# Kernel tuning notes

Hardware: AMD Instinct MI355X
Metric: run time of the kernel (lower is better)

Reference implementation:

```python
import jax, jax.numpy as jnp
import numpy as np

D = 768
N_GROUPS = 4
KEYS_PER_Q = 4 * 196  # 784


def setup_inputs() -> dict:
    key = jax.random.key(0)
    ks = jax.random.split(key, 6)
    scale = 0.02
    return {
        "LR_image": jax.random.normal(ks[0], (N_GROUPS, 32, D), jnp.float32),
        "HR_image": jax.random.normal(ks[1], (N_GROUPS, 32 * KEYS_PER_Q, D), jnp.float32),
        "Wq": jax.random.normal(ks[2], (D, D), jnp.float32) * scale,
        "bq": jnp.zeros((D,), jnp.float32),
        "Wk": jax.random.normal(ks[3], (D, D), jnp.float32) * scale,
        "bk": jnp.zeros((D,), jnp.float32),
        "Wv": jax.random.normal(ks[4], (D, D), jnp.float32) * scale,
        "bv": jnp.zeros((D,), jnp.float32),
        "Wo": jax.random.normal(ks[5], (D, D), jnp.float32) * scale,
        "bo": jnp.zeros((D,), jnp.float32),
        "gamma": jnp.ones((D,), jnp.float32),
        "beta": jnp.zeros((D,), jnp.float32),
    }


def reference(LR_image, HR_image, Wq, bq, Wk, bk, Wv, bv, Wo, bo, gamma, beta):
    d = LR_image.shape[-1]
    # version == 2 reshapes from the original forward
    lr = LR_image.reshape(1, -1, 32, 1, d)            # [1, N, 32, 1, D]
    hr = HR_image.reshape(1, -1, 32, KEYS_PER_Q, d)   # [1, N, 32, 784, D]
    q = lr @ Wq.T + bq                                # [1, N, 32, 1, D]
    k = hr @ Wk.T + bk                                # [1, N, 32, 784, D]
    v = hr @ Wv.T + bv
    # single-head attention; query_len == 1, key_len == 784
    scores = jnp.einsum('bnsqd,bnskd->bnsqk', q, k) / jnp.sqrt(jnp.float32(d))
    p = jax.nn.softmax(scores, axis=-1)               # dropout = identity (eval)
    x = jnp.einsum('bnsqk,bnskd->bnsqd', p, v)        # [1, N, 32, 1, D]
    x = x.reshape(1, -1, d)                           # [1, N*32, D]
    q = q.reshape(1, -1, d)
    x = x @ Wo.T + bo
    y = q + x                                         # residual (dropout_2 = identity)
    mu = jnp.mean(y, axis=-1, keepdims=True)
    var = jnp.mean((y - mu) ** 2, axis=-1, keepdims=True)
    return (y - mu) * jax.lax.rsqrt(var + 1e-5) * gamma + beta
```

## Files before the change

kernel.cpp:

```cpp
#include <hip/hip_runtime.h>
#include <math.h>

#define D 768
#define DF2 384
#define DF4 192
#define NQ 128
#define KPQ 784
#define NCHUNK 16
#define KCHUNK 49

#define EXP2F(x) __builtin_amdgcn_exp2f(x)

__device__ __forceinline__ float dot4f(const float4 a, const float4 b) {
    return a.x * b.x + a.y * b.y + a.z * b.z + a.w * b.w;
}

__global__ __launch_bounds__(256) void k_tr(const float* __restrict__ Wq,
                                            const float* __restrict__ Wv,
                                            const float* __restrict__ Wo,
                                            float* __restrict__ WqT,
                                            float* __restrict__ WvT,
                                            float* __restrict__ WoT) {
    __shared__ float t[64][65];
    const float* src;
    float* dst;
    if (blockIdx.y == 0)      { src = Wq; dst = WqT; }
    else if (blockIdx.y == 1) { src = Wv; dst = WvT; }
    else                      { src = Wo; dst = WoT; }
    const int tr = blockIdx.x / 12, tc = blockIdx.x % 12;
    const int r0 = tr * 64, c0 = tc * 64;
    const int lr = threadIdx.x >> 6, lc = threadIdx.x & 63;
#pragma unroll
    for (int i = 0; i < 16; ++i)
        t[lr + i * 4][lc] = src[(size_t)(r0 + lr + i * 4) * D + c0 + lc];
    __syncthreads();
#pragma unroll
    for (int i = 0; i < 16; ++i)
        dst[(size_t)(c0 + lr + i * 4) * D + r0 + lc] = t[lc][lr + i * 4];
}

template <bool BIAS, bool RES, bool SCALE>
__global__ __launch_bounds__(512) void k_gemm2(const float* __restrict__ A,
                                               const float2* __restrict__ W2,
                                               const float2* __restrict__ bias2,
                                               const float2* __restrict__ res2,
                                               float2* __restrict__ Out2) {
    __shared__ float2 part[8][4][64];
    const int ct  = blockIdx.x % 6;
    const int q0  = (blockIdx.x / 6) * 4;
    const int tid = threadIdx.x;
    const int ds  = __builtin_amdgcn_readfirstlane(tid >> 6);
    const int c2  = tid & 63;
    const int e2  = ct * 64 + c2;
    const float* a0 = A + (size_t)q0 * D;
    const float* a1 = a0 + D;
    const float* a2 = a1 + D;
    const float* a3 = a2 + D;
    float2 acc0 = {0.f, 0.f}, acc1 = {0.f, 0.f}, acc2 = {0.f, 0.f}, acc3 = {0.f, 0.f};
    const int dbase = ds * 96;
#pragma unroll 8
    for (int i = 0; i < 96; ++i) {
        const int d = dbase + i;
        const float2 wv = W2[(size_t)d * DF2 + e2];
        const float x0 = a0[d], x1 = a1[d], x2 = a2[d], x3 = a3[d];
        acc0.x = fmaf(x0, wv.x, acc0.x); acc0.y = fmaf(x0, wv.y, acc0.y);
        acc1.x = fmaf(x1, wv.x, acc1.x); acc1.y = fmaf(x1, wv.y, acc1.y);
        acc2.x = fmaf(x2, wv.x, acc2.x); acc2.y = fmaf(x2, wv.y, acc2.y);
        acc3.x = fmaf(x3, wv.x, acc3.x); acc3.y = fmaf(x3, wv.y, acc3.y);
    }
    part[ds][0][c2] = acc0;
    part[ds][1][c2] = acc1;
    part[ds][2][c2] = acc2;
    part[ds][3][c2] = acc3;
    __syncthreads();
    if (tid < 256) {
        const int q = tid >> 6, c = tid & 63;
        float2 s = {0.f, 0.f};
#pragma unroll
        for (int p = 0; p < 8; ++p) {
            s.x += part[p][q][c].x;
            s.y += part[p][q][c].y;
        }
        if (BIAS) {
            const float2 b = bias2[ct * 64 + c];
            s.x += b.x; s.y += b.y;
        }
        if (RES) {
            const float2 r = res2[(size_t)(q0 + q) * DF2 + ct * 64 + c];
            s.x += r.x; s.y += r.y;
        }
        if (SCALE) {
            const float rsd2 = 0.036084391824351615f * 1.4426950408889634f;
            s.x *= rsd2; s.y *= rsd2;
        }
        Out2[(size_t)(q0 + q) * DF2 + ct * 64 + c] = s;
    }
}

__global__ __launch_bounds__(256) void k_flash(const float4* __restrict__ HR,
                                               const float4* __restrict__ qt,
                                               float4* __restrict__ Cpart,
                                               float* __restrict__ Lp) {
    const int b     = blockIdx.x;
    const int qi    = b >> 4;
    const int chunk = b & 15;
    const size_t rowbase = (size_t)qi * KPQ + (size_t)chunk * KCHUNK;
    const int tid  = threadIdx.x;
    const int w    = tid >> 6;
    const int lane = tid & 63;

    const float4 qa = qt[qi * DF4 + lane];
    const float4 qb = qt[qi * DF4 + lane + 64];
    const float4 qc = qt[qi * DF4 + lane + 128];

    float l = 0.f;
    float4 c0 = make_float4(0.f, 0.f, 0.f, 0.f);
    float4 c1 = make_float4(0.f, 0.f, 0.f, 0.f);
    float4 c2 = make_float4(0.f, 0.f, 0.f, 0.f);

    int j = w;
    while (j + 12 < KCHUNK) {
        const float4* rA = HR + (rowbase + (size_t)j) * DF4;
        const float4* rB = HR + (rowbase + (size_t)(j + 4)) * DF4;
        const float4* rF = HR + (rowbase + (size_t)(j + 8)) * DF4;
        const float4* rG = HR + (rowbase + (size_t)(j + 12)) * DF4;
        const float4 a0 = rA[lane], a1 = rA[lane + 64], a2 = rA[lane + 128];
        const float4 b0 = rB[lane], b1 = rB[lane + 64], b2 = rB[lane + 128];
        const float4 f0 = rF[lane], f1 = rF[lane + 64], f2 = rF[lane + 128];
        const float4 g0 = rG[lane], g1 = rG[lane + 64], g2 = rG[lane + 128];
        float p1 = dot4f(qa, a0) + dot4f(qb, a1) + dot4f(qc, a2);
        float p2 = dot4f(qa, b0) + dot4f(qb, b1) + dot4f(qc, b2);
        float p3 = dot4f(qa, f0) + dot4f(qb, f1) + dot4f(qc, f2);
        float p4 = dot4f(qa, g0) + dot4f(qb, g1) + dot4f(qc, g2);
#pragma unroll
        for (int off = 32; off; off >>= 1) {
            p1 += __shfl_xor(p1, off, 64);
            p2 += __shfl_xor(p2, off, 64);
            p3 += __shfl_xor(p3, off, 64);
            p4 += __shfl_xor(p4, off, 64);
        }
        const float e1 = EXP2F(p1);
        const float e2 = EXP2F(p2);
        const float e3 = EXP2F(p3);
        const float e4 = EXP2F(p4);
        l += (e1 + e2) + (e3 + e4);
        c0.x = fmaf(e1, a0.x, fmaf(e2, b0.x, fmaf(e3, f0.x, fmaf(e4, g0.x, c0.x))));
        c0.y = fmaf(e1, a0.y, fmaf(e2, b0.y, fmaf(e3, f0.y, fmaf(e4, g0.y, c0.y))));
        c0.z = fmaf(e1, a0.z, fmaf(e2, b0.z, fmaf(e3, f0.z, fmaf(e4, g0.z, c0.z))));
        c0.w = fmaf(e1, a0.w, fmaf(e2, b0.w, fmaf(e3, f0.w, fmaf(e4, g0.w, c0.w))));
        c1.x = fmaf(e1, a1.x, fmaf(e2, b1.x, fmaf(e3, f1.x, fmaf(e4, g1.x, c1.x))));
        c1.y = fmaf(e1, a1.y, fmaf(e2, b1.y, fmaf(e3, f1.y, fmaf(e4, g1.y, c1.y))));
        c1.z = fmaf(e1, a1.z, fmaf(e2, b1.z, fmaf(e3, f1.z, fmaf(e4, g1.z, c1.z))));
        c1.w = fmaf(e1, a1.w, fmaf(e2, b1.w, fmaf(e3, f1.w, fmaf(e4, g1.w, c1.w))));
        c2.x = fmaf(e1, a2.x, fmaf(e2, b2.x, fmaf(e3, f2.x, fmaf(e4, g2.x, c2.x))));
        c2.y = fmaf(e1, a2.y, fmaf(e2, b2.y, fmaf(e3, f2.y, fmaf(e4, g2.y, c2.y))));
        c2.z = fmaf(e1, a2.z, fmaf(e2, b2.z, fmaf(e3, f2.z, fmaf(e4, g2.z, c2.z))));
        c2.w = fmaf(e1, a2.w, fmaf(e2, b2.w, fmaf(e3, f2.w, fmaf(e4, g2.w, c2.w))));
        j += 16;
    }
    while (j < KCHUNK) {
        const float4* rA = HR + (rowbase + (size_t)j) * DF4;
        const float4 a0 = rA[lane], a1 = rA[lane + 64], a2 = rA[lane + 128];
        float p1 = dot4f(qa, a0) + dot4f(qb, a1) + dot4f(qc, a2);
#pragma unroll
        for (int off = 32; off; off >>= 1) p1 += __shfl_xor(p1, off, 64);
        const float e1 = EXP2F(p1);
        l += e1;
        c0.x = fmaf(e1, a0.x, c0.x); c0.y = fmaf(e1, a0.y, c0.y);
        c0.z = fmaf(e1, a0.z, c0.z); c0.w = fmaf(e1, a0.w, c0.w);
        c1.x = fmaf(e1, a1.x, c1.x); c1.y = fmaf(e1, a1.y, c1.y);
        c1.z = fmaf(e1, a1.z, c1.z); c1.w = fmaf(e1, a1.w, c1.w);
        c2.x = fmaf(e1, a2.x, c2.x); c2.y = fmaf(e1, a2.y, c2.y);
        c2.z = fmaf(e1, a2.z, c2.z); c2.w = fmaf(e1, a2.w, c2.w);
        j += 4;
    }

    __shared__ __align__(16) float4 c_lds[4][DF4];
    __shared__ float l_lds[4];
    c_lds[w][lane]       = c0;
    c_lds[w][lane + 64]  = c1;
    c_lds[w][lane + 128] = c2;
    if (lane == 0) l_lds[w] = l;
    __syncthreads();

    if (tid < DF4) {
        float4 cc = make_float4(0.f, 0.f, 0.f, 0.f);
#pragma unroll
        for (int p = 0; p < 4; ++p) {
            const float4 cv = c_lds[p][tid];
            cc.x += cv.x; cc.y += cv.y; cc.z += cv.z; cc.w += cv.w;
        }
        Cpart[(size_t)b * DF4 + tid] = cc;
        if (tid == 0) Lp[b] = l_lds[0] + l_lds[1] + l_lds[2] + l_lds[3];
    }
}

__global__ __launch_bounds__(192) void k_combine(const float4* __restrict__ Cpart,
                                                 const float* __restrict__ Lp,
                                                 float4* __restrict__ Cn) {
    const int qi = blockIdx.x;
    const int f  = threadIdx.x;
    float L = 0.f;
#pragma unroll
    for (int p = 0; p < NCHUNK; ++p) L += Lp[qi * NCHUNK + p];
    float4 c = make_float4(0.f, 0.f, 0.f, 0.f);
#pragma unroll
    for (int p = 0; p < NCHUNK; ++p) {
        const float4 v = Cpart[(size_t)(qi * NCHUNK + p) * DF4 + f];
        c.x += v.x; c.y += v.y; c.z += v.z; c.w += v.w;
    }
    const float inv = 1.f / L;
    c.x *= inv; c.y *= inv; c.z *= inv; c.w *= inv;
    Cn[(size_t)qi * DF4 + f] = c;
}

__global__ __launch_bounds__(256) void k_ln(const float* __restrict__ y,
                                            const float* __restrict__ gamma,
                                            const float* __restrict__ beta,
                                            float* __restrict__ out) {
    __shared__ float sp[4], ssp[4];
    const int qi = blockIdx.x;
    const int tid = threadIdx.x, w = tid >> 6, lane = tid & 63;
    const float* yr = y + (size_t)qi * D;
    const float v0 = yr[tid], v1 = yr[tid + 256], v2 = yr[tid + 512];
    float s  = v0 + v1 + v2;
    float ss = v0 * v0 + v1 * v1 + v2 * v2;
#pragma unroll
    for (int off = 32; off; off >>= 1) {
        s  += __shfl_xor(s, off, 64);
        ss += __shfl_xor(ss, off, 64);
    }
    if (lane == 0) { sp[w] = s; ssp[w] = ss; }
    __syncthreads();
    s  = sp[0] + sp[1] + sp[2] + sp[3];
    ss = ssp[0] + ssp[1] + ssp[2] + ssp[3];
    const float mu  = s * (1.f / 768.f);
    const float var = ss * (1.f / 768.f) - mu * mu;
    const float rs  = rsqrtf(var + 1e-5f);
    float* o = out + (size_t)qi * D;
    o[tid]       = (v0 - mu) * rs * gamma[tid]       + beta[tid];
    o[tid + 256] = (v1 - mu) * rs * gamma[tid + 256] + beta[tid + 256];
    o[tid + 512] = (v2 - mu) * rs * gamma[tid + 512] + beta[tid + 512];
}

extern "C" void kernel_launch(void* const* d_in, const int* in_sizes, int n_in,
                              void* d_out, int out_size, void* d_ws, size_t ws_size,
                              hipStream_t stream) {
    const float* LR    = (const float*)d_in[0];
    const float* HR    = (const float*)d_in[1];
    const float* Wq    = (const float*)d_in[2];
    const float* bq    = (const float*)d_in[3];
    const float* Wk    = (const float*)d_in[4];
    const float* Wv    = (const float*)d_in[6];
    const float* bv    = (const float*)d_in[7];
    const float* Wo    = (const float*)d_in[8];
    const float* bo    = (const float*)d_in[9];
    const float* gamma = (const float*)d_in[10];
    const float* beta  = (const float*)d_in[11];
    float* out = (float*)d_out;

    float* ws = (float*)d_ws;
    float* WqT   = ws;
    float* WvT   = ws + 589824;
    float* WoT   = ws + 1179648;
    float* qbuf  = ws + 1769472;
    float* qtbuf = ws + 1867776;
    float* Cpart = ws + 1966080;
    float* Lp    = ws + 3538944;
    float* Cn    = ws + 3540992;
    float* Xbuf  = ws + 3639296;
    float* ybuf  = ws + 3737600;

    k_tr<<<dim3(144, 3), 256, 0, stream>>>(Wq, Wv, Wo, WqT, WvT, WoT);
    k_gemm2<true, false, false><<<192, 512, 0, stream>>>(
        LR, (const float2*)WqT, (const float2*)bq, nullptr, (float2*)qbuf);
    k_gemm2<false, false, true><<<192, 512, 0, stream>>>(
        qbuf, (const float2*)Wk, nullptr, nullptr, (float2*)qtbuf);
    k_flash<<<NQ * NCHUNK, 256, 0, stream>>>((const float4*)HR, (const float4*)qtbuf,
                                             (float4*)Cpart, Lp);
    k_combine<<<NQ, 192, 0, stream>>>((const float4*)Cpart, Lp, (float4*)Cn);
    k_gemm2<true, false, false><<<192, 512, 0, stream>>>(
        Cn, (const float2*)WvT, (const float2*)bv, nullptr, (float2*)Xbuf);
    k_gemm2<true, true, false><<<192, 512, 0, stream>>>(
        Xbuf, (const float2*)WoT, (const float2*)bo, (const float2*)qbuf, (float2*)ybuf);
    k_ln<<<NQ, 256, 0, stream>>>(ybuf, gamma, beta, out);
}
```

Measured before the change: 103.3 us.

## Split each wavefront into four 16-lane groups processing separate key rows

Restructures the flash attention kernel so each 64-lane wavefront handles four key rows at once, with each 16-lane group owning a full 768-wide row (12 float4 per lane). The dot-product reduction shrinks from a 6-step to a 4-step shuffle, and per-row partial accumulators are reduced through a larger LDS buffer. This cuts cross-lane shuffle work and exposes more independent loads per lane, at the cost of higher register pressure (12 q and 12 accumulator float4s plus 12 loaded values), masked work on tail rows, and more LDS traffic in the final reduction.

```diff
diff --git a/kernel.cpp b/kernel.cpp
--- a/kernel.cpp
+++ b/kernel.cpp
@@ -108,88 +108,60 @@
     const int tid  = threadIdx.x;
     const int w    = tid >> 6;
     const int lane = tid & 63;
-
-    const float4 qa = qt[qi * DF4 + lane];
-    const float4 qb = qt[qi * DF4 + lane + 64];
-    const float4 qc = qt[qi * DF4 + lane + 128];
+    const int g    = lane >> 4;
+    const int lg   = lane & 15;
+
+    float4 qf[12];
+#pragma unroll
+    for (int k = 0; k < 12; ++k) qf[k] = qt[qi * DF4 + lg + 16 * k];
 
     float l = 0.f;
-    float4 c0 = make_float4(0.f, 0.f, 0.f, 0.f);
-    float4 c1 = make_float4(0.f, 0.f, 0.f, 0.f);
-    float4 c2 = make_float4(0.f, 0.f, 0.f, 0.f);
-
-    int j = w;
-    while (j + 12 < KCHUNK) {
-        const float4* rA = HR + (rowbase + (size_t)j) * DF4;
-        const float4* rB = HR + (rowbase + (size_t)(j + 4)) * DF4;
-        const float4* rF = HR + (rowbase + (size_t)(j + 8)) * DF4;
-        const float4* rG = HR + (rowbase + (size_t)(j + 12)) * DF4;
-        const float4 a0 = rA[lane], a1 = rA[lane + 64], a2 = rA[lane + 128];
-        const float4 b0 = rB[lane], b1 = rB[lane + 64], b2 = rB[lane + 128];
-        const float4 f0 = rF[lane], f1 = rF[lane + 64], f2 = rF[lane + 128];
-        const float4 g0 = rG[lane], g1 = rG[lane + 64], g2 = rG[lane + 128];
-        float p1 = dot4f(qa, a0) + dot4f(qb, a1) + dot4f(qc, a2);
-        float p2 = dot4f(qa, b0) + dot4f(qb, b1) + dot4f(qc, b2);
-        float p3 = dot4f(qa, f0) + dot4f(qb, f1) + dot4f(qc, f2);
-        float p4 = dot4f(qa, g0) + dot4f(qb, g1) + dot4f(qc, g2);
-#pragma unroll
-        for (int off = 32; off; off >>= 1) {
-            p1 += __shfl_xor(p1, off, 64);
-            p2 += __shfl_xor(p2, off, 64);
-            p3 += __shfl_xor(p3, off, 64);
-            p4 += __shfl_xor(p4, off, 64);
-        }
-        const float e1 = EXP2F(p1);
-        const float e2 = EXP2F(p2);
-        const float e3 = EXP2F(p3);
-        const float e4 = EXP2F(p4);
-        l += (e1 + e2) + (e3 + e4);
-        c0.x = fmaf(e1, a0.x, fmaf(e2, b0.x, fmaf(e3, f0.x, fmaf(e4, g0.x, c0.x))));
-        c0.y = fmaf(e1, a0.y, fmaf(e2, b0.y, fmaf(e3, f0.y, fmaf(e4, g0.y, c0.y))));
-        c0.z = fmaf(e1, a0.z, fmaf(e2, b0.z, fmaf(e3, f0.z, fmaf(e4, g0.z, c0.z))));
-        c0.w = fmaf(e1, a0.w, fmaf(e2, b0.w, fmaf(e3, f0.w, fmaf(e4, g0.w, c0.w))));
-        c1.x = fmaf(e1, a1.x, fmaf(e2, b1.x, fmaf(e3, f1.x, fmaf(e4, g1.x, c1.x))));
-        c1.y = fmaf(e1, a1.y, fmaf(e2, b1.y, fmaf(e3, f1.y, fmaf(e4, g1.y, c1.y))));
-        c1.z = fmaf(e1, a1.z, fmaf(e2, b1.z, fmaf(e3, f1.z, fmaf(e4, g1.z, c1.z))));
-        c1.w = fmaf(e1, a1.w, fmaf(e2, b1.w, fmaf(e3, f1.w, fmaf(e4, g1.w, c1.w))));
-        c2.x = fmaf(e1, a2.x, fmaf(e2, b2.x, fmaf(e3, f2.x, fmaf(e4, g2.x, c2.x))));
-        c2.y = fmaf(e1, a2.y, fmaf(e2, b2.y, fmaf(e3, f2.y, fmaf(e4, g2.y, c2.y))));
-        c2.z = fmaf(e1, a2.z, fmaf(e2, b2.z, fmaf(e3, f2.z, fmaf(e4, g2.z, c2.z))));
-        c2.w = fmaf(e1, a2.w, fmaf(e2, b2.w, fmaf(e3, f2.w, fmaf(e4, g2.w, c2.w))));
-        j += 16;
-    }
-    while (j < KCHUNK) {
-        const float4* rA = HR + (rowbase + (size_t)j) * DF4;
-        const float4 a0 = rA[lane], a1 = rA[lane + 64], a2 = rA[lane + 128];
-        float p1 = dot4f(qa, a0) + dot4f(qb, a1) + dot4f(qc, a2);
-#pragma unroll
-        for (int off = 32; off; off >>= 1) p1 += __shfl_xor(p1, off, 64);
-        const float e1 = EXP2F(p1);
-        l += e1;
-        c0.x = fmaf(e1, a0.x, c0.x); c0.y = fmaf(e1, a0.y, c0.y);
-        c0.z = fmaf(e1, a0.z, c0.z); c0.w = fmaf(e1, a0.w, c0.w);
-        c1.x = fmaf(e1, a1.x, c1.x); c1.y = fmaf(e1, a1.y, c1.y);
-        c1.z = fmaf(e1, a1.z, c1.z); c1.w = fmaf(e1, a1.w, c1.w);
-        c2.x = fmaf(e1, a2.x, c2.x); c2.y = fmaf(e1, a2.y, c2.y);
-        c2.z = fmaf(e1, a2.z, c2.z); c2.w = fmaf(e1, a2.w, c2.w);
-        j += 4;
-    }
-
-    __shared__ __align__(16) float4 c_lds[4][DF4];
+    float4 acc[12];
+#pragma unroll
+    for (int k = 0; k < 12; ++k) acc[k] = make_float4(0.f, 0.f, 0.f, 0.f);
+
+    for (int j = 4 * w; j < KCHUNK; j += 16) {
+        const int row  = j + g;
+        const bool ok  = row < KCHUNK;
+        const int srow = ok ? row : (KCHUNK - 1);
+        const float4* rp = HR + (rowbase + (size_t)srow) * DF4;
+        float4 v[12];
+#pragma unroll
+        for (int k = 0; k < 12; ++k) v[k] = rp[lg + 16 * k];
+        float p = 0.f;
+#pragma unroll
+        for (int k = 0; k < 12; ++k) p += dot4f(qf[k], v[k]);
+#pragma unroll
+        for (int off = 1; off < 16; off <<= 1) p += __shfl_xor(p, off, 64);
+        const float e = ok ? EXP2F(p) : 0.f;
+        l += e;
+#pragma unroll
+        for (int k = 0; k < 12; ++k) {
+            acc[k].x = fmaf(e, v[k].x, acc[k].x);
+            acc[k].y = fmaf(e, v[k].y, acc[k].y);
+            acc[k].z = fmaf(e, v[k].z, acc[k].z);
+            acc[k].w = fmaf(e, v[k].w, acc[k].w);
+        }
+    }
+    l += __shfl_xor(l, 16, 64);
+    l += __shfl_xor(l, 32, 64);
+
+    __shared__ __align__(16) float4 c_lds[4][4][DF4];
     __shared__ float l_lds[4];
-    c_lds[w][lane]       = c0;
-    c_lds[w][lane + 64]  = c1;
-    c_lds[w][lane + 128] = c2;
+#pragma unroll
+    for (int k = 0; k < 12; ++k) c_lds[w][g][lg + 16 * k] = acc[k];
     if (lane == 0) l_lds[w] = l;
     __syncthreads();
 
     if (tid < DF4) {
         float4 cc = make_float4(0.f, 0.f, 0.f, 0.f);
 #pragma unroll
-        for (int p = 0; p < 4; ++p) {
-            const float4 cv = c_lds[p][tid];
-            cc.x += cv.x; cc.y += cv.y; cc.z += cv.z; cc.w += cv.w;
-        }
+        for (int ww = 0; ww < 4; ++ww)
+#pragma unroll
+            for (int gg = 0; gg < 4; ++gg) {
+                const float4 cv = c_lds[ww][gg][tid];
+                cc.x += cv.x; cc.y += cv.y; cc.z += cv.z; cc.w += cv.w;
+            }
         Cpart[(size_t)b * DF4 + tid] = cc;
         if (tid == 0) Lp[b] = l_lds[0] + l_lds[1] + l_lds[2] + l_lds[3];
     }
```

Result: no change. 104.9 us (+1.5%).
